# Kernel tuning notes

Hardware: AMD Instinct MI355X
Metric: run time of the kernel (lower is better)

Reference implementation:

```python
import jax, jax.numpy as jnp
from jax import lax
import numpy as np

EPS = 1e-5  # BatchNorm eps (inference mode; dropouts are identity in eval)


def _proj(img, w, g, b, m, v, stride):
    """All-heads Conv2d(3x3, no bias) + BatchNorm (inference) fused across heads.
    img: [B, Cin, H, W]; w: [heads, Cout, Cin, 3, 3]; g/b/m/v: [heads, Cout].
    Returns [B, heads, Cout, N'] (channels-first token layout)."""
    heads, Cout, Cin = w.shape[0], w.shape[1], w.shape[2]
    y = lax.conv_general_dilated(
        img, w.reshape(heads * Cout, Cin, 3, 3),
        window_strides=(stride, stride), padding=[(1, 1), (1, 1)],
        dimension_numbers=('NCHW', 'OIHW', 'NCHW'))
    B = y.shape[0]
    N = y.shape[2] * y.shape[3]
    y = y.reshape(B, heads, Cout, N)
    scale = g / jnp.sqrt(v + EPS)               # [heads, Cout]
    shift = b - m * scale
    return y * scale[None, :, :, None] + shift[None, :, :, None]


def reference(x, y, w_conv, bn_gamma, bn_beta, bn_mean, bn_var, w_out1, w_out2, h, w):
    B, N, C = x.shape
    xi = x.reshape(B, h, w, C).transpose(0, 3, 1, 2)  # b (h w) c -> b c h w
    yi = y.reshape(B, h, w, C).transpose(0, 3, 1, 2)
    scale_attn = C ** -0.5

    def P(i, img, stride):
        return _proj(img, w_conv[i], bn_gamma[i], bn_beta[i], bn_mean[i], bn_var[i], stride)

    # torch: query1(x), query2(y), key1(y), key2(x), value1(y), value2(x)
    Q1 = P(0, xi, 2)  # [B,h,C,Nq]
    Q2 = P(1, yi, 2)
    K1 = P(2, yi, 2)
    K2 = P(3, xi, 2)
    V1 = P(4, yi, 1)  # [B,h,C,Nv]
    V2 = P(5, xi, 1)

    # channel-attention: scores are [B, heads, C, C], softmax over last axis
    s1 = jnp.einsum('bhcn,bhdn->bhcd', Q2, K1) * scale_attn
    s2 = jnp.einsum('bhcn,bhdn->bhcd', Q1, K2) * scale_attn
    p1 = jax.nn.softmax(s1, axis=-1)
    p2 = jax.nn.softmax(s2, axis=-1)

    # context [B,heads,C,Nv] -> mean over heads -> [B,Nv,C]
    c1 = jnp.einsum('bhcd,bhdn->bhcn', p1, V1).mean(axis=1).transpose(0, 2, 1)
    c2 = jnp.einsum('bhcd,bhdn->bhcn', p2, V2).mean(axis=1).transpose(0, 2, 1)

    o1 = c1 @ w_out1.T  # Linear(dim_in, dim_out, bias=False)
    o2 = c2 @ w_out2.T
    return o1, o2


def setup_inputs() -> dict:
    B, C, HEADS, H, W = 8, 256, 4, 64, 64
    key = jax.random.key(0)
    ks = jax.random.split(key, 9)
    conv_std = 1.0 / np.sqrt(C * 9)
    lin_std = 1.0 / np.sqrt(C)
    return {
        'x': jax.random.normal(ks[0], (B, H * W, C), jnp.float32),
        'y': jax.random.normal(ks[1], (B, H * W, C), jnp.float32),
        'w_conv': jax.random.normal(ks[2], (6, HEADS, C, C, 3, 3), jnp.float32) * conv_std,
        'bn_gamma': jax.random.uniform(ks[3], (6, HEADS, C), jnp.float32, 0.5, 1.5),
        'bn_beta': jax.random.normal(ks[4], (6, HEADS, C), jnp.float32) * 0.1,
        'bn_mean': jax.random.normal(ks[5], (6, HEADS, C), jnp.float32) * 0.1,
        'bn_var': jax.random.uniform(ks[6], (6, HEADS, C), jnp.float32, 0.5, 1.5),
        'w_out1': jax.random.normal(ks[7], (C, C), jnp.float32) * lin_std,
        'w_out2': jax.random.normal(ks[8], (C, C), jnp.float32) * lin_std,
        'h': H,
        'w': W,
    }
```

## Files before the change

kernel.cpp:

```cpp
#include <hip/hip_runtime.h>
#include <stdint.h>

typedef __bf16 bf16_t;
typedef __bf16 bf16x8 __attribute__((ext_vector_type(8)));
typedef float f32x4 __attribute__((ext_vector_type(4)));

#define EPSBN 1e-5f

#define OFF_XP   ((size_t)0)
#define SZ_IMG   ((size_t)8*4356*256*2)
#define OFF_YP   (OFF_XP + SZ_IMG)
#define OFF_WQS  (OFF_YP + SZ_IMG)
#define SZ_WQS   ((size_t)4*1024*2304*2)
#define OFF_WVT  (OFF_WQS + SZ_WQS)
#define SZ_WVT   ((size_t)2*2304*1024*2)
#define OFF_W1B  (OFF_WVT + SZ_WVT)
#define SZ_WO    ((size_t)65536*2)
#define OFF_W2B  (OFF_W1B + SZ_WO)
#define OFF_SHQ  (OFF_W2B + SZ_WO)
#define SZ_SHQ   ((size_t)4096*4)
#define OFF_SHV  (OFF_SHQ + SZ_SHQ)
#define SZ_SHV   ((size_t)2048*4)
#define OFF_QK   (OFF_SHV + SZ_SHV)
#define SZ_QK    ((size_t)4*8*1024*1024*2)
#define OFF_S    (OFF_QK + SZ_QK)
#define SZ_S     ((size_t)2*8*4*65536*4)
#define OFF_PT   (OFF_S + SZ_S)
#define SZ_PT    ((size_t)2*8*4*65536*2)
#define OFF_A1   (OFF_PT + SZ_PT)
#define SZ_A1    ((size_t)2*8*256*1024*2)
#define OFF_WEFF (OFF_A1 + SZ_A1)
#define SZ_WEFF  ((size_t)2*8*256*2304*2)
#define OFF_BIAS (OFF_WEFF + SZ_WEFF)
#define SZ_BIAS  ((size_t)2*8*256*4)
#define WS_NEED  (OFF_BIAS + SZ_BIAS)

__device__ __forceinline__ void gload16(const bf16_t* g, bf16_t* l) {
  __builtin_amdgcn_global_load_lds(
      (const __attribute__((address_space(1))) void*)g,
      (__attribute__((address_space(3))) void*)l,
      16, 0, 0);
}

__device__ __forceinline__ int lb_off0() { return ((threadIdx.x >> 6)    ) * 512; }
__device__ __forceinline__ int lb_off1() { return ((threadIdx.x >> 6) + 4) * 512; }

#define SBAR0 __builtin_amdgcn_sched_barrier(0)

template<int BSRC>
__device__ __forceinline__ void gemm_core(
    const bf16_t* __restrict__ A, int ldA,
    const bf16_t* __restrict__ B, int ldB,
    int m0, int n0, int KT, f32x4 acc[4][4])
{
  __shared__ bf16_t lA[2][4096];
  __shared__ bf16_t lB[2][4096];
  const int tid  = threadIdx.x;
  const int lane = tid & 63;
  const int wv   = tid >> 6;
  const int wr   = wv >> 1, wc = wv & 1;
  const int r4   = lane >> 2;
  const int k8   = (lane & 3) * 8;

  const bf16_t* gA0 = A + (size_t)(m0 + (wv    )*16 + r4) * ldA + k8;
  const bf16_t* gA1 = A + (size_t)(m0 + (wv + 4)*16 + r4) * ldA + k8;
  const int la0 = (wv    ) * 512;
  const int la1 = (wv + 4) * 512;
  const bf16_t* gB0 = B + (size_t)(n0 + (wv    )*16 + r4) * ldB + k8;
  const bf16_t* gB1 = B + (size_t)(n0 + (wv + 4)*16 + r4) * ldB + k8;
  (void)BSRC;

#pragma unroll
  for (int i = 0; i < 4; ++i)
#pragma unroll
    for (int j = 0; j < 4; ++j)
      acc[i][j] = f32x4{0.f, 0.f, 0.f, 0.f};

  const int lr = lane & 15;
  const int lk = (lane >> 4) * 8;
  int aidx[4], bidx[4];
#pragma unroll
  for (int f = 0; f < 4; ++f) {
    aidx[f] = (wr*64 + f*16 + lr)*32 + lk;
    bidx[f] = (wc*64 + f*16 + lr)*32 + lk;
  }

  auto stage = [&](int bufp, int kt) {
    const int kb = kt * 32;
    gload16(gA0 + kb, &lA[bufp][la0]);
    gload16(gA1 + kb, &lA[bufp][la1]);
    gload16(gB0 + kb, &lB[bufp][lb_off0()]);
    gload16(gB1 + kb, &lB[bufp][lb_off1()]);
  };

  stage(0, 0);
  __syncthreads();
  int buf = 0;
  for (int kt = 0; kt < KT; ++kt) {
    if (kt + 1 < KT) stage(buf ^ 1, kt + 1);
    bf16x8 av[4], bvv[4];
#pragma unroll
    for (int f = 0; f < 4; ++f) av[f]  = *(const bf16x8*)&lA[buf][aidx[f]];
#pragma unroll
    for (int f = 0; f < 4; ++f) bvv[f] = *(const bf16x8*)&lB[buf][bidx[f]];
#pragma unroll
    for (int i = 0; i < 4; ++i)
#pragma unroll
      for (int j = 0; j < 4; ++j)
        acc[i][j] = __builtin_amdgcn_mfma_f32_16x16x32_bf16(av[i], bvv[j], acc[i][j], 0, 0, 0);
    __syncthreads();
    buf ^= 1;
  }
}

template<int STRIDE>
__device__ __forceinline__ void conv_m201_core(
    const bf16_t* __restrict__ A, const bf16_t* __restrict__ img,
    int m0, int n0, f32x4 acc[8][4])
{
  __shared__ bf16_t lA[2][2][8192];
  __shared__ bf16_t lB[2][2][8192];
  const int tid  = threadIdx.x;
  const int lane = tid & 63;
  const int w    = tid >> 6;
  const int wm   = w >> 2;
  const int wn   = w & 3;
  const int wh   = wn >> 1;
  const int wn1  = wn & 1;

#pragma unroll
  for (int f = 0; f < 8; ++f)
#pragma unroll
    for (int c = 0; c < 4; ++c)
      acc[f][c] = f32x4{0.f, 0.f, 0.f, 0.f};

  const int srow = tid >> 3;
  const int swz  = ((tid & 7) ^ (srow & 7)) * 8;
  const bf16_t* gAsrc = A + (size_t)(m0 + srow) * 2304 + swz;
  const bf16_t* gBsrc[4];
#pragma unroll
  for (int h = 0; h < 2; ++h)
#pragma unroll
    for (int c = 0; c < 2; ++c) {
      const int tok = n0 + h*128 + c*64 + srow;
      int px;
      if (STRIDE == 1) px = (tok >> 6)*66 + (tok & 63);
      else             px = ((tok >> 5)*2)*66 + (tok & 31)*2;
      gBsrc[h*2 + c] = img + (size_t)px*256 + swz;
    }

  auto stageA = [&](int T1, int h) {
    bf16_t* dst = &lA[T1 & 1][h][0] + tid*8;
    const bf16_t* src = gAsrc + (size_t)(h*128)*2304 + T1*64;
    gload16(src, dst);
    gload16(src + (size_t)64*2304, dst + 4096);
  };
  auto stageB = [&](int T1, int h) {
    const int tap = T1 >> 2;
    const int ky  = (tap >= 6) ? 2 : ((tap >= 3) ? 1 : 0);
    const int kx  = tap - ky*3;
    const int ps  = (ky*66 + kx)*256 + (T1 & 3)*64;
    bf16_t* dst = &lB[T1 & 1][h][0] + tid*8;
    gload16(gBsrc[h*2 + 0] + ps, dst);
    gload16(gBsrc[h*2 + 1] + ps, dst + 4096);
  };

  const int rb  = (lane & 15) * 64;
  const int l7  = lane & 7;
  const int g4  = lane >> 4;
  int rs[2];
  rs[0] = ((    g4) ^ l7) * 8;
  rs[1] = ((4 + g4) ^ l7) * 8;

  stageA(0, 0); stageB(0, 0); stageA(0, 1); stageB(0, 1);
  SBAR0;
  asm volatile("s_waitcnt vmcnt(0)" ::: "memory");
  SBAR0;
  __builtin_amdgcn_s_barrier();

  for (int T = 0; T < 36; ++T) {
    const int buf = T & 1;
    const bf16_t* pa = &lA[buf][wm][0];
    const bf16_t* pb = &lB[buf][wh][0];
    bf16x8 av[4][2], bv[2][2];

#define CONV_PHASE(MH, NH, RA, STAGE_STMT, VM0, LG8)                          \
    do {                                                                      \
      _Pragma("unroll") for (int j = 0; j < 2; ++j)                           \
        _Pragma("unroll") for (int kh = 0; kh < 2; ++kh)                      \
          bv[j][kh] = *(const bf16x8*)(pb + (wn1*4096 + ((NH)*2+j)*1024 + rb + rs[kh])); \
      if (RA) {                                                               \
        _Pragma("unroll") for (int i = 0; i < 4; ++i)                         \
          _Pragma("unroll") for (int kh = 0; kh < 2; ++kh)                    \
            av[i][kh] = *(const bf16x8*)(pa + (((MH)*4+i)*1024 + rb + rs[kh])); \
      }                                                                       \
      STAGE_STMT;                                                             \
      SBAR0;                                                                  \
      if (VM0) { asm volatile("s_waitcnt vmcnt(0)" ::: "memory"); }           \
      if (LG8) { asm volatile("s_waitcnt lgkmcnt(8)" ::: "memory"); }         \
      __builtin_amdgcn_s_barrier();                                           \
      asm volatile("s_waitcnt lgkmcnt(0)" ::: "memory");                      \
      SBAR0;                                                                  \
      __builtin_amdgcn_s_setprio(1);                                          \
      _Pragma("unroll") for (int i = 0; i < 4; ++i)                           \
        _Pragma("unroll") for (int j = 0; j < 2; ++j)                         \
          _Pragma("unroll") for (int kh = 0; kh < 2; ++kh)                    \
            acc[(MH)*4+i][(NH)*2+j] = __builtin_amdgcn_mfma_f32_16x16x32_bf16(\
                av[i][kh], bv[j][kh], acc[(MH)*4+i][(NH)*2+j], 0, 0, 0);      \
      __builtin_amdgcn_s_setprio(0);                                          \
      __builtin_amdgcn_s_barrier();                                           \
    } while (0)

    const bool nt = (T + 1 < 36);
    CONV_PHASE(0, 0, 1, if (nt) { stageA(T+1, 0); stageB(T+1, 0); }, 0, 1);
    CONV_PHASE(0, 1, 0, if (nt) { stageA(T+1, 1); stageB(T+1, 1); }, 0, 0);
    CONV_PHASE(1, 0, 1, (void)0, 0, 1);
    CONV_PHASE(1, 1, 0, (void)0, 1, 0);
#undef CONV_PHASE
  }
}

__global__ __launch_bounds__(512, 1) void k_conv_qk7(const bf16_t* __restrict__ wqs,
    const bf16_t* __restrict__ xp, const bf16_t* __restrict__ yp,
    bf16_t* __restrict__ qk, const float* __restrict__ shq)
{
  const int n  = blockIdx.x;
  const int b  = n & 7;
  const int r1 = n >> 3;
  const int ci = r1 & 3;
  const int r2 = r1 >> 2;
  const int nt = r2 & 3;
  const int mt = r2 >> 2;
  const int m0 = mt*256, n0 = nt*256;
  const bf16_t* A = wqs + (size_t)ci * 1024 * 2304;
  const bf16_t* img = (((ci == 0) | (ci == 3)) ? xp : yp) + (size_t)b*4356*256;
  f32x4 acc[8][4];
  conv_m201_core<2>(A, img, m0, n0, acc);

  bf16_t* out = qk + (size_t)(ci*8 + b) * 1024 * 1024;
  const float* sh = shq + ci*1024;
  const int lane = threadIdx.x & 63, w = threadIdx.x >> 6;
  const int wm = w >> 2, wn = w & 3;
#pragma unroll
  for (int f = 0; f < 8; ++f) {
    const int row0 = m0 + wm*128 + f*16 + ((lane >> 4) << 2);
    const f32x4 s4 = *(const f32x4*)&sh[row0];
#pragma unroll
    for (int c = 0; c < 4; ++c) {
      const int col = n0 + wn*64 + c*16 + (lane & 15);
#pragma unroll
      for (int r = 0; r < 4; ++r)
        out[(size_t)(row0 + r)*1024 + col] = (bf16_t)(acc[f][c][r] + s4[r]);
    }
  }
}

__global__ __launch_bounds__(512, 1) void k_conv_out7(const bf16_t* __restrict__ weff,
    const bf16_t* __restrict__ xp, const bf16_t* __restrict__ yp,
    const float* __restrict__ bias, float* __restrict__ dout)
{
  const int n  = blockIdx.x;
  const int b  = n & 7;
  const int r1 = n >> 3;
  const int br = r1 & 1;
  const int nt = r1 >> 1;
  const int n0 = nt*256;
  const bf16_t* A = weff + (size_t)(br*8 + b)*589824;
  const bf16_t* img = ((br == 0) ? yp : xp) + (size_t)b*4356*256;
  f32x4 acc[8][4];
  conv_m201_core<1>(A, img, 0, n0, acc);

  float* outp = dout + (size_t)br*8388608 + (size_t)b*1048576;
  const float* bp = bias + (size_t)(br*8 + b)*256;
  const int lane = threadIdx.x & 63, w = threadIdx.x >> 6;
  const int wm = w >> 2, wn = w & 3;
#pragma unroll
  for (int f = 0; f < 8; ++f) {
    const int e0 = wm*128 + f*16 + ((lane >> 4) << 2);
    const f32x4 bv4 = *(const f32x4*)&bp[e0];
#pragma unroll
    for (int c = 0; c < 4; ++c) {
      const int tok = n0 + wn*64 + c*16 + (lane & 15);
      f32x4 v = acc[f][c] + bv4;
      *(f32x4*)&outp[(size_t)tok*256 + e0] = v;
    }
  }
}

__global__ __launch_bounds__(256) void k_pack(const float* __restrict__ x, const float* __restrict__ y,
                                              bf16_t* __restrict__ xp, bf16_t* __restrict__ yp)
{
  const int p  = blockIdx.x;
  const int b  = blockIdx.y;
  const int im = blockIdx.z;
  const int c  = threadIdx.x;
  const int i = p / 66, j = p - i*66;
  const float* src = im ? y : x;
  bf16_t* dst = im ? yp : xp;
  float v = 0.f;
  if (i >= 1 && i <= 64 && j >= 1 && j <= 64)
    v = src[((size_t)b*4096 + (size_t)(i-1)*64 + (j-1))*256 + c];
  dst[((size_t)b*4356 + p)*256 + c] = (bf16_t)v;
}

__global__ __launch_bounds__(256) void k_prep_wq(const float* __restrict__ wcv,
    const float* __restrict__ g, const float* __restrict__ be,
    const float* __restrict__ mu, const float* __restrict__ va,
    bf16_t* __restrict__ wqs, float* __restrict__ shq)
{
  const int blk = blockIdx.x;
  __shared__ float lw[2304];
  const float* src = wcv + (size_t)blk * 2304;
  for (int t = threadIdx.x; t < 2304; t += 256) lw[t] = src[t];
  const float sc = g[blk] * rsqrtf(va[blk] + EPSBN);
  if (threadIdx.x == 0) shq[blk] = be[blk] - mu[blk]*sc;
  __syncthreads();
  bf16_t* dst = wqs + (size_t)blk * 2304;
  for (int t = threadIdx.x; t < 2304; t += 256) {
    const int tap = t >> 8, c = t & 255;
    dst[t] = (bf16_t)(lw[c*9 + tap] * sc);
  }
}

__global__ __launch_bounds__(256) void k_prep_wv(const float* __restrict__ wcv,
    const float* __restrict__ g, const float* __restrict__ va,
    bf16_t* __restrict__ wvT)
{
  const int cch = blockIdx.x;
  const int h = blockIdx.y >> 2, dc = blockIdx.y & 3;
  const int br = blockIdx.z;
  __shared__ float lw[64][72];
  __shared__ float lsc[64];
  const int ci = 4 + br;
  const int c0 = cch*8, d0 = dc*64;
  for (int e = threadIdx.x; e < 64*72; e += 256) {
    const int dd = e / 72, q = e - dd*72;
    lw[dd][q] = wcv[(size_t)(ci*1024 + h*256 + d0 + dd)*2304 + c0*9 + q];
  }
  if (threadIdx.x < 64) {
    const int bnIdx = ci*1024 + h*256 + d0 + threadIdx.x;
    lsc[threadIdx.x] = g[bnIdx] * rsqrtf(va[bnIdx] + EPSBN);
  }
  __syncthreads();
  for (int e = threadIdx.x; e < 72*64; e += 256) {
    const int kq = e >> 6, dd = e & 63;
    const int cc = kq / 9, tap = kq - cc*9;
    const int kp = tap*256 + c0 + cc;
    wvT[(size_t)br*2359296 + (size_t)kp*1024 + h*256 + d0 + dd] =
        (bf16_t)(lw[dd][cc*9 + tap] * lsc[dd]);
  }
}

__global__ __launch_bounds__(256) void k_small(const float* __restrict__ w1, const float* __restrict__ w2,
    const float* __restrict__ g, const float* __restrict__ be,
    const float* __restrict__ mu, const float* __restrict__ va,
    bf16_t* __restrict__ w1b, bf16_t* __restrict__ w2b, float* __restrict__ shv)
{
  const int idx = blockIdx.x*256 + threadIdx.x;
  if (idx < 65536) {
    w1b[idx] = (bf16_t)w1[idx];
  } else if (idx < 131072) {
    w2b[idx - 65536] = (bf16_t)w2[idx - 65536];
  } else if (idx < 133120) {
    const int t = idx - 131072;
    const int bnIdx = 4096 + t;
    const float sc = g[bnIdx] * rsqrtf(va[bnIdx] + EPSBN);
    shv[t] = be[bnIdx] - mu[bnIdx]*sc;
  }
}

__global__ __launch_bounds__(256) void k_gemm_s(const bf16_t* __restrict__ qk, float* __restrict__ sb)
{
  const int bx = blockIdx.x, by = blockIdx.y, br = blockIdx.z;
  const int mt = bx >> 1, nt = bx & 1;
  const int b = by >> 2, h = by & 3;
  const int ai = (br == 0) ? 1 : 0;
  const int bi = (br == 0) ? 2 : 3;
  const bf16_t* A  = qk + ((size_t)(ai*8 + b)*1024 + h*256) * 1024;
  const bf16_t* Bp = qk + ((size_t)(bi*8 + b)*1024 + h*256) * 1024;
  f32x4 acc[4][4];
  gemm_core<0>(A, 1024, Bp, 1024, mt*128, nt*128, 32, acc);

  float* out = sb + ((size_t)(br*8 + b)*4 + h) * 65536;
  const int lane = threadIdx.x & 63, wv = threadIdx.x >> 6;
  const int wr = wv >> 1, wc = wv & 1;
#pragma unroll
  for (int i = 0; i < 4; ++i) {
    const int row0 = mt*128 + wr*64 + i*16 + ((lane >> 4) << 2);
#pragma unroll
    for (int j = 0; j < 4; ++j) {
      const int col = nt*128 + wc*64 + j*16 + (lane & 15);
#pragma unroll
      for (int r = 0; r < 4; ++r)
        out[(size_t)(row0 + r)*256 + col] = acc[i][j][r];
    }
  }
}

__global__ __launch_bounds__(256) void k_softmax(const float* __restrict__ sb, bf16_t* __restrict__ pt)
{
  const int cc = blockIdx.x;
  const int bh = blockIdx.y;
  const int br = blockIdx.z;
  const size_t base = ((size_t)br*32 + bh) * 65536;
  __shared__ bf16_t lp[32][256];
  const int tid = threadIdx.x, lane = tid & 63, wv = tid >> 6;
  for (int r = 0; r < 8; ++r) {
    const int row = wv*8 + r;
    const float* srow = sb + base + (size_t)(cc*32 + row)*256;
    f32x4 v = ((const f32x4*)srow)[lane];
    v *= 0.0625f;
    float m = fmaxf(fmaxf(v[0], v[1]), fmaxf(v[2], v[3]));
#pragma unroll
    for (int o = 32; o; o >>= 1) m = fmaxf(m, __shfl_xor(m, o));
    const float e0 = __expf(v[0]-m), e1 = __expf(v[1]-m), e2 = __expf(v[2]-m), e3 = __expf(v[3]-m);
    float s = e0+e1+e2+e3;
#pragma unroll
    for (int o = 32; o; o >>= 1) s += __shfl_xor(s, o);
    const float inv = 0.25f / s;
    lp[row][lane*4+0] = (bf16_t)(e0*inv);
    lp[row][lane*4+1] = (bf16_t)(e1*inv);
    lp[row][lane*4+2] = (bf16_t)(e2*inv);
    lp[row][lane*4+3] = (bf16_t)(e3*inv);
  }
  __syncthreads();
  bf16_t* dst = pt + base;
  for (int it = 0; it < 32; ++it) {
    const int idx = it*256 + tid;
    const int d = idx >> 5, c = idx & 31;
    dst[(size_t)d*256 + cc*32 + c] = lp[c][d];
  }
}

__global__ __launch_bounds__(256) void k_gemm_a(const bf16_t* __restrict__ w1b, const bf16_t* __restrict__ w2b,
    const bf16_t* __restrict__ pt, bf16_t* __restrict__ a1)
{
  const int bx = blockIdx.x, by = blockIdx.y, br = blockIdx.z;
  const int mt = bx >> 1, nt = bx & 1;
  const int b = by >> 2, h = by & 3;
  const bf16_t* A  = br ? w2b : w1b;
  const bf16_t* Bp = pt + ((size_t)(br*8 + b)*4 + h) * 65536;
  f32x4 acc[4][4];
  gemm_core<0>(A, 256, Bp, 256, mt*128, nt*128, 8, acc);

  bf16_t* out = a1 + (size_t)(br*8 + b)*262144 + h*256;
  const int lane = threadIdx.x & 63, wv = threadIdx.x >> 6;
  const int wr = wv >> 1, wc = wv & 1;
#pragma unroll
  for (int i = 0; i < 4; ++i) {
    const int row0 = mt*128 + wr*64 + i*16 + ((lane >> 4) << 2);
#pragma unroll
    for (int j = 0; j < 4; ++j) {
      const int col = nt*128 + wc*64 + j*16 + (lane & 15);
#pragma unroll
      for (int r = 0; r < 4; ++r)
        out[(size_t)(row0 + r)*1024 + col] = (bf16_t)acc[i][j][r];
    }
  }
}

__global__ __launch_bounds__(256) void k_bias(const bf16_t* __restrict__ a1,
    const float* __restrict__ shv, float* __restrict__ bias)
{
  const int wv = threadIdx.x >> 6, lane = threadIdx.x & 63;
  const int e = blockIdx.x*4 + wv;
  const int b = blockIdx.y, br = blockIdx.z;
  const bf16_t* row = a1 + ((size_t)(br*8 + b)*256 + e)*1024;
  const float* sv = shv + br*1024;
  float acc = 0.f;
#pragma unroll
  for (int t = 0; t < 16; ++t) {
    const int idx = t*64 + lane;
    acc += (float)row[idx] * sv[idx];
  }
#pragma unroll
  for (int o = 32; o; o >>= 1) acc += __shfl_xor(acc, o);
  if (lane == 0) bias[(size_t)(br*8 + b)*256 + e] = acc;
}

__global__ __launch_bounds__(256) void k_gemm_weff(const bf16_t* __restrict__ a1,
    const bf16_t* __restrict__ wvT, bf16_t* __restrict__ weff)
{
  const int bx = blockIdx.x, b = blockIdx.y, br = blockIdx.z;
  const int mt = bx / 18, nt = bx - mt*18;
  const bf16_t* A  = a1 + (size_t)(br*8 + b)*262144;
  const bf16_t* Bp = wvT + (size_t)br*2359296;
  f32x4 acc[4][4];
  gemm_core<0>(A, 1024, Bp, 1024, mt*128, nt*128, 32, acc);

  bf16_t* out = weff + (size_t)(br*8 + b)*589824;
  const int lane = threadIdx.x & 63, wv = threadIdx.x >> 6;
  const int wr = wv >> 1, wc = wv & 1;
#pragma unroll
  for (int i = 0; i < 4; ++i) {
    const int row0 = mt*128 + wr*64 + i*16 + ((lane >> 4) << 2);
#pragma unroll
    for (int j = 0; j < 4; ++j) {
      const int col = nt*128 + wc*64 + j*16 + (lane & 15);
#pragma unroll
      for (int r = 0; r < 4; ++r)
        out[(size_t)(row0 + r)*2304 + col] = (bf16_t)acc[i][j][r];
    }
  }
}

extern "C" void kernel_launch(void* const* d_in, const int* in_sizes, int n_in,
                              void* d_out, int out_size, void* d_ws, size_t ws_size,
                              hipStream_t stream)
{
  (void)in_sizes; (void)n_in; (void)out_size;
  const float* x   = (const float*)d_in[0];
  const float* y   = (const float*)d_in[1];
  const float* wcv = (const float*)d_in[2];
  const float* bg  = (const float*)d_in[3];
  const float* bb  = (const float*)d_in[4];
  const float* bm  = (const float*)d_in[5];
  const float* bvv = (const float*)d_in[6];
  const float* w1  = (const float*)d_in[7];
  const float* w2  = (const float*)d_in[8];
  float* out = (float*)d_out;
  char* ws = (char*)d_ws;
  if (ws_size < WS_NEED) return;

  bf16_t* xp   = (bf16_t*)(ws + OFF_XP);
  bf16_t* yp   = (bf16_t*)(ws + OFF_YP);
  bf16_t* wqs  = (bf16_t*)(ws + OFF_WQS);
  bf16_t* wvT  = (bf16_t*)(ws + OFF_WVT);
  bf16_t* w1b  = (bf16_t*)(ws + OFF_W1B);
  bf16_t* w2b  = (bf16_t*)(ws + OFF_W2B);
  float*  shq  = (float*)(ws + OFF_SHQ);
  float*  shv  = (float*)(ws + OFF_SHV);
  bf16_t* qk   = (bf16_t*)(ws + OFF_QK);
  float*  sb   = (float*)(ws + OFF_S);
  bf16_t* pt   = (bf16_t*)(ws + OFF_PT);
  bf16_t* a1   = (bf16_t*)(ws + OFF_A1);
  bf16_t* weff = (bf16_t*)(ws + OFF_WEFF);
  float*  bias = (float*)(ws + OFF_BIAS);

  k_pack     <<<dim3(4356, 8, 2), 256, 0, stream>>>(x, y, xp, yp);
  k_prep_wq  <<<dim3(4096), 256, 0, stream>>>(wcv, bg, bb, bm, bvv, wqs, shq);
  k_prep_wv  <<<dim3(32, 16, 2), 256, 0, stream>>>(wcv, bg, bvv, wvT);
  k_small    <<<dim3(520), 256, 0, stream>>>(w1, w2, bg, bb, bm, bvv, w1b, w2b, shv);
  k_conv_qk7 <<<dim3(512), 512, 0, stream>>>(wqs, xp, yp, qk, shq);
  k_gemm_s   <<<dim3(4, 32, 2), 256, 0, stream>>>(qk, sb);
  k_softmax  <<<dim3(8, 32, 2), 256, 0, stream>>>(sb, pt);
  k_gemm_a   <<<dim3(4, 32, 2), 256, 0, stream>>>(w1b, w2b, pt, a1);
  k_bias     <<<dim3(64, 8, 2), 256, 0, stream>>>(a1, shv, bias);
  k_gemm_weff<<<dim3(36, 8, 2), 256, 0, stream>>>(a1, wvT, weff);
  k_conv_out7<<<dim3(256), 512, 0, stream>>>(weff, xp, yp, bias, out);
}
```

Before: 375.0 us.

## Cache B fragments across conv phases and vectorize the input packing kernel

The conv main loop now keeps both halves of the B fragments in registers (bvs[2]) so that phases 3 and 4 reuse them instead of reloading from LDS. The fourth phase issues no LDS reads at all, and the third phase waits with a looser lgkmcnt. Separately, k_pack handles four pixels per block, with 64 threads each loading a float4 and storing four bf16 as one 64-bit write, which cuts block count and memory instructions. The register caching raises VGPR pressure in a kernel already bounded at 512 threads.

```diff
diff --git a/kernel.cpp b/kernel.cpp
--- a/kernel.cpp
+++ b/kernel.cpp
@@ -182,41 +182,92 @@
     const int buf = T & 1;
     const bf16_t* pa = &lA[buf][wm][0];
     const bf16_t* pb = &lB[buf][wh][0];
-    bf16x8 av[4][2], bv[2][2];
-
-#define CONV_PHASE(MH, NH, RA, STAGE_STMT, VM0, LG8)                          \
-    do {                                                                      \
-      _Pragma("unroll") for (int j = 0; j < 2; ++j)                           \
-        _Pragma("unroll") for (int kh = 0; kh < 2; ++kh)                      \
-          bv[j][kh] = *(const bf16x8*)(pb + (wn1*4096 + ((NH)*2+j)*1024 + rb + rs[kh])); \
-      if (RA) {                                                               \
-        _Pragma("unroll") for (int i = 0; i < 4; ++i)                         \
-          _Pragma("unroll") for (int kh = 0; kh < 2; ++kh)                    \
-            av[i][kh] = *(const bf16x8*)(pa + (((MH)*4+i)*1024 + rb + rs[kh])); \
-      }                                                                       \
-      STAGE_STMT;                                                             \
-      SBAR0;                                                                  \
-      if (VM0) { asm volatile("s_waitcnt vmcnt(0)" ::: "memory"); }           \
-      if (LG8) { asm volatile("s_waitcnt lgkmcnt(8)" ::: "memory"); }         \
-      __builtin_amdgcn_s_barrier();                                           \
-      asm volatile("s_waitcnt lgkmcnt(0)" ::: "memory");                      \
-      SBAR0;                                                                  \
-      __builtin_amdgcn_s_setprio(1);                                          \
-      _Pragma("unroll") for (int i = 0; i < 4; ++i)                           \
-        _Pragma("unroll") for (int j = 0; j < 2; ++j)                         \
-          _Pragma("unroll") for (int kh = 0; kh < 2; ++kh)                    \
-            acc[(MH)*4+i][(NH)*2+j] = __builtin_amdgcn_mfma_f32_16x16x32_bf16(\
-                av[i][kh], bv[j][kh], acc[(MH)*4+i][(NH)*2+j], 0, 0, 0);      \
-      __builtin_amdgcn_s_setprio(0);                                          \
-      __builtin_amdgcn_s_barrier();                                           \
-    } while (0)
-
+    bf16x8 av[4][2], bvs[2][2][2];
     const bool nt = (T + 1 < 36);
-    CONV_PHASE(0, 0, 1, if (nt) { stageA(T+1, 0); stageB(T+1, 0); }, 0, 1);
-    CONV_PHASE(0, 1, 0, if (nt) { stageA(T+1, 1); stageB(T+1, 1); }, 0, 0);
-    CONV_PHASE(1, 0, 1, (void)0, 0, 1);
-    CONV_PHASE(1, 1, 0, (void)0, 1, 0);
-#undef CONV_PHASE
+
+#pragma unroll
+    for (int j = 0; j < 2; ++j)
+#pragma unroll
+      for (int kh = 0; kh < 2; ++kh)
+        bvs[0][j][kh] = *(const bf16x8*)(pb + (wn1*4096 + j*1024 + rb + rs[kh]));
+#pragma unroll
+    for (int i = 0; i < 4; ++i)
+#pragma unroll
+      for (int kh = 0; kh < 2; ++kh)
+        av[i][kh] = *(const bf16x8*)(pa + (i*1024 + rb + rs[kh]));
+    if (nt) { stageA(T+1, 0); stageB(T+1, 0); }
+    SBAR0;
+    asm volatile("s_waitcnt lgkmcnt(8)" ::: "memory");
+    __builtin_amdgcn_s_barrier();
+    asm volatile("s_waitcnt lgkmcnt(0)" ::: "memory");
+    SBAR0;
+    __builtin_amdgcn_s_setprio(1);
+#pragma unroll
+    for (int i = 0; i < 4; ++i)
+#pragma unroll
+      for (int j = 0; j < 2; ++j)
+#pragma unroll
+        for (int kh = 0; kh < 2; ++kh)
+          acc[i][j] = __builtin_amdgcn_mfma_f32_16x16x32_bf16(av[i][kh], bvs[0][j][kh], acc[i][j], 0, 0, 0);
+    __builtin_amdgcn_s_setprio(0);
+    __builtin_amdgcn_s_barrier();
+
+#pragma unroll
+    for (int j = 0; j < 2; ++j)
+#pragma unroll
+      for (int kh = 0; kh < 2; ++kh)
+        bvs[1][j][kh] = *(const bf16x8*)(pb + (wn1*4096 + (2+j)*1024 + rb + rs[kh]));
+    if (nt) { stageA(T+1, 1); stageB(T+1, 1); }
+    SBAR0;
+    __builtin_amdgcn_s_barrier();
+    asm volatile("s_waitcnt lgkmcnt(0)" ::: "memory");
+    SBAR0;
+    __builtin_amdgcn_s_setprio(1);
+#pragma unroll
+    for (int i = 0; i < 4; ++i)
+#pragma unroll
+      for (int j = 0; j < 2; ++j)
+#pragma unroll
+        for (int kh = 0; kh < 2; ++kh)
+          acc[i][2+j] = __builtin_amdgcn_mfma_f32_16x16x32_bf16(av[i][kh], bvs[1][j][kh], acc[i][2+j], 0, 0, 0);
+    __builtin_amdgcn_s_setprio(0);
+    __builtin_amdgcn_s_barrier();
+
+#pragma unroll
+    for (int i = 0; i < 4; ++i)
+#pragma unroll
+      for (int kh = 0; kh < 2; ++kh)
+        av[i][kh] = *(const bf16x8*)(pa + ((4+i)*1024 + rb + rs[kh]));
+    SBAR0;
+    asm volatile("s_waitcnt lgkmcnt(4)" ::: "memory");
+    __builtin_amdgcn_s_barrier();
+    asm volatile("s_waitcnt lgkmcnt(0)" ::: "memory");
+    SBAR0;
+    __builtin_amdgcn_s_setprio(1);
+#pragma unroll
+    for (int i = 0; i < 4; ++i)
+#pragma unroll
+      for (int j = 0; j < 2; ++j)
+#pragma unroll
+        for (int kh = 0; kh < 2; ++kh)
+          acc[4+i][j] = __builtin_amdgcn_mfma_f32_16x16x32_bf16(av[i][kh], bvs[0][j][kh], acc[4+i][j], 0, 0, 0);
+    __builtin_amdgcn_s_setprio(0);
+    __builtin_amdgcn_s_barrier();
+
+    SBAR0;
+    asm volatile("s_waitcnt vmcnt(0)" ::: "memory");
+    SBAR0;
+    __builtin_amdgcn_s_barrier();
+    __builtin_amdgcn_s_setprio(1);
+#pragma unroll
+    for (int i = 0; i < 4; ++i)
+#pragma unroll
+      for (int j = 0; j < 2; ++j)
+#pragma unroll
+        for (int kh = 0; kh < 2; ++kh)
+          acc[4+i][2+j] = __builtin_amdgcn_mfma_f32_16x16x32_bf16(av[i][kh], bvs[1][j][kh], acc[4+i][2+j], 0, 0, 0);
+    __builtin_amdgcn_s_setprio(0);
+    __builtin_amdgcn_s_barrier();
   }
 }
 
@@ -290,17 +341,19 @@
 __global__ __launch_bounds__(256) void k_pack(const float* __restrict__ x, const float* __restrict__ y,
                                               bf16_t* __restrict__ xp, bf16_t* __restrict__ yp)
 {
-  const int p  = blockIdx.x;
-  const int b  = blockIdx.y;
-  const int im = blockIdx.z;
-  const int c  = threadIdx.x;
-  const int i = p / 66, j = p - i*66;
+  const int t   = threadIdx.x;
+  const int pix = blockIdx.x*4 + (t >> 6);
+  const int c4  = (t & 63) * 4;
+  const int b   = blockIdx.y;
+  const int im  = blockIdx.z;
+  const int i = pix / 66, j = pix - i*66;
   const float* src = im ? y : x;
   bf16_t* dst = im ? yp : xp;
-  float v = 0.f;
+  float4 v = make_float4(0.f, 0.f, 0.f, 0.f);
   if (i >= 1 && i <= 64 && j >= 1 && j <= 64)
-    v = src[((size_t)b*4096 + (size_t)(i-1)*64 + (j-1))*256 + c];
-  dst[((size_t)b*4356 + p)*256 + c] = (bf16_t)v;
+    v = *(const float4*)&src[((size_t)b*4096 + (size_t)(i-1)*64 + (j-1))*256 + c4];
+  bf16_t o4[4] = {(bf16_t)v.x, (bf16_t)v.y, (bf16_t)v.z, (bf16_t)v.w};
+  *(uint64_t*)&dst[((size_t)b*4356 + pix)*256 + c4] = *(const uint64_t*)o4;
 }
 
 __global__ __launch_bounds__(256) void k_prep_wq(const float* __restrict__ wcv,
@@ -537,7 +590,7 @@
   bf16_t* weff = (bf16_t*)(ws + OFF_WEFF);
   float*  bias = (float*)(ws + OFF_BIAS);
 
-  k_pack     <<<dim3(4356, 8, 2), 256, 0, stream>>>(x, y, xp, yp);
+  k_pack     <<<dim3(1089, 8, 2), 256, 0, stream>>>(x, y, xp, yp);
   k_prep_wq  <<<dim3(4096), 256, 0, stream>>>(wcv, bg, bb, bm, bvv, wqs, shq);
   k_prep_wv  <<<dim3(32, 16, 2), 256, 0, stream>>>(wcv, bg, bvv, wvT);
   k_small    <<<dim3(520), 256, 0, stream>>>(w1, w2, bg, bb, bm, bvv, w1b, w2b, shv);
```

New measurement: 351.1 us. 6.4% less time.
